# Optimization experiments

Measured on AMD Instinct MI355X. Metric: run time of the kernel, lower is better.

The kernel has to match this reference:

```python
import jax, jax.numpy as jnp
import numpy as np
import math

B, S, E = 4, 2048, 1024


def setup_inputs() -> dict:
    key = jax.random.key(0)
    ks = jax.random.split(key, 7)
    w_scale = 1.0 / math.sqrt(E)
    x = jax.random.normal(ks[0], (B, S, E), dtype=jnp.float32)
    Wq = jax.random.normal(ks[1], (E, E), dtype=jnp.float32) * w_scale
    bq = jax.random.normal(ks[2], (E,), dtype=jnp.float32) * 0.01
    Wk = jax.random.normal(ks[3], (E, E), dtype=jnp.float32) * w_scale
    bk = jax.random.normal(ks[4], (E,), dtype=jnp.float32) * 0.01
    Wv = jax.random.normal(ks[5], (E, E), dtype=jnp.float32) * w_scale
    bv = jax.random.normal(ks[6], (E,), dtype=jnp.float32) * 0.01
    # causal mask: True = attend, False = masked (mask == 0 -> -inf)
    mask = jnp.broadcast_to(jnp.tril(jnp.ones((S, S), dtype=bool)), (B, S, S))
    return {"x": x, "Wq": Wq, "bq": bq, "Wk": Wk, "bk": bk, "Wv": Wv, "bv": bv, "mask": mask}


def reference(x, Wq, bq, Wk, bk, Wv, bv, mask):
    # nn.Linear stores weight as [out, in]: y = x @ W.T + b
    Q = jnp.einsum("bse,oe->bso", x, Wq) + bq
    K = jnp.einsum("bse,oe->bso", x, Wk) + bk
    V = jnp.einsum("bse,oe->bso", x, Wv) + bv
    scale = math.sqrt(E)
    scores = jnp.einsum("bqe,bke->bqk", Q, K) / scale  # [B,S,S]
    scores = jnp.where(mask, scores, -jnp.inf)
    attn = jax.nn.softmax(scores, axis=-1)
    out = jnp.einsum("bqk,bke->bqe", attn, V)  # [B,S,E]
    return out
```

## Files before the change

kernel.cpp:

```cpp
#include <hip/hip_runtime.h>
#include <stdint.h>

typedef unsigned short u16;
typedef __attribute__((ext_vector_type(8))) short bf16x8;
typedef __attribute__((ext_vector_type(4))) float f32x4;

#define MFMA16(a, b, c) __builtin_amdgcn_mfma_f32_16x16x32_bf16((a), (b), (c), 0, 0, 0)

#define MASKVAL (-1.0e30f)

#define WAITV(N) asm volatile("s_waitcnt vmcnt(" #N ")" ::: "memory")
#define LGKM0()  asm volatile("s_waitcnt lgkmcnt(0)" ::: "memory")
#define SBAR()   __builtin_amdgcn_s_barrier()

__device__ __forceinline__ u16 f2bf(float f) {
  union { float f; uint32_t u; } v; v.f = f;
  uint32_t u = v.u;
  u += 0x7fffu + ((u >> 16) & 1u);
  return (u16)(u >> 16);
}
__device__ __forceinline__ void async16(const void* g, void* l) {
  __builtin_amdgcn_global_load_lds(
      (const __attribute__((address_space(1))) unsigned int*)g,
      (__attribute__((address_space(3))) unsigned int*)l, 16, 0, 0);
}

__global__ __launch_bounds__(256) void conv_kernel(
    const float* __restrict__ x,  const float* __restrict__ wq,
    const float* __restrict__ wk, const float* __restrict__ wv,
    u16* __restrict__ xb, u16* __restrict__ wb, int do_wv)
{
  const int NX = 1 << 20;
  const int NW = 1 << 17;
  const int total = NX + NW * (do_wv ? 3 : 2);
  for (int i = blockIdx.x * 256 + threadIdx.x; i < total; i += gridDim.x * 256) {
    const float* src; u16* dst;
    if (i < NX) {
      src = x + (size_t)i * 8;
      const int m = i >> 7, k8 = i & 127;
      dst = xb + (size_t)m * 2048 + 1024 + k8 * 8;
    } else {
      const int j = i - NX;
      const int wsel = j >> 17;
      const int jj = j & (NW - 1);
      const float* W = (wsel == 0) ? wq : (wsel == 1) ? wk : wv;
      const int zoff = (wsel == 0) ? 0 : (wsel == 1) ? (2 << 20) : (1 << 20);
      src = W + (size_t)jj * 8;
      dst = wb + zoff + jj * 8;
    }
    float4 f0 = *(const float4*)src;
    float4 f1 = *(const float4*)(src + 4);
    ushort4 h0, h1;
    h0.x = f2bf(f0.x); h0.y = f2bf(f0.y); h0.z = f2bf(f0.z); h0.w = f2bf(f0.w);
    h1.x = f2bf(f1.x); h1.y = f2bf(f1.y); h1.z = f2bf(f1.z); h1.w = f2bf(f1.w);
    *(ushort4*)dst = h0;
    *(ushort4*)(dst + 4) = h1;
  }
}

template <int BMODE>
__global__ __launch_bounds__(256) void gemm_kernel(
    const u16* __restrict__ xb,
    const u16* __restrict__ wb,
    const float* __restrict__ wv_f,
    const float* __restrict__ bq, const float* __restrict__ bk,
    const float* __restrict__ bv,
    u16* __restrict__ q_out, u16* __restrict__ vt_out, u16* __restrict__ k_out,
    int zbase, int zmul)
{
  const int z = zbase + (int)blockIdx.z * zmul;
  __shared__ u16 lA[2][128 * 32];
  __shared__ u16 lB[2][128 * 32];

  const int m0 = blockIdx.x * 128, n0 = blockIdx.y * 128;
  const int tid = threadIdx.x, lane = tid & 63, w = tid >> 6;
  const int quad = lane >> 4, l15 = lane & 15;
  const int wr = (w >> 1) * 64, wc = (w & 1) * 64;

  const u16* wz = wb + ((size_t)z << 20);
  const float* bias = (z == 0) ? bq : (z == 1) ? bv : bk;

  const int sr  = lane >> 2;
  const int ssw = (lane >> 3) & 3;
  const int c16s = (lane & 3) ^ ssw;

  auto stageA = [&](int kk, int bbuf) {
    const int k0 = kk * 32;
#pragma unroll
    for (int i = 0; i < 2; ++i) {
      const int r = w * 32 + i * 16 + sr;
      async16(&xb[(size_t)(m0 + r) * 2048 + 1024 + k0 + c16s * 8],
              &lA[bbuf][w * 1024 + i * 512]);
    }
  };
  auto stageB = [&](int kk, int bbuf) {
    const int k0 = kk * 32;
#pragma unroll
    for (int i = 0; i < 2; ++i) {
      const int r = w * 32 + i * 16 + sr;
      async16(&wz[(size_t)(n0 + r) * 1024 + k0 + c16s * 8],
              &lB[bbuf][w * 1024 + i * 512]);
    }
  };

  float4 bfr[4];
  const int br = tid >> 1;
  const int bcb = (tid & 1) * 2;
  const int bs = (br >> 1) & 3;
  auto loadB = [&](int kk) {
    const float* p = &wv_f[(size_t)(n0 + br) * 1024 + kk * 32 + bcb * 8];
    bfr[0] = ((const float4*)p)[0];
    bfr[1] = ((const float4*)p)[1];
    bfr[2] = ((const float4*)p)[2];
    bfr[3] = ((const float4*)p)[3];
  };
  auto writeB = [&](int bbuf) {
    ushort4 h[4];
#pragma unroll
    for (int g = 0; g < 4; ++g) {
      h[g].x = f2bf(bfr[g].x); h[g].y = f2bf(bfr[g].y);
      h[g].z = f2bf(bfr[g].z); h[g].w = f2bf(bfr[g].w);
    }
    const int p0 = (bcb + 0) ^ bs, p1 = (bcb + 1) ^ bs;
    *(ushort4*)&lB[bbuf][br * 32 + p0 * 8]     = h[0];
    *(ushort4*)&lB[bbuf][br * 32 + p0 * 8 + 4] = h[1];
    *(ushort4*)&lB[bbuf][br * 32 + p1 * 8]     = h[2];
    *(ushort4*)&lB[bbuf][br * 32 + p1 * 8 + 4] = h[3];
  };

  f32x4 zero4 = {0.f, 0.f, 0.f, 0.f};
  f32x4 acc[4][4];
#pragma unroll
  for (int i = 0; i < 4; ++i)
#pragma unroll
    for (int j = 0; j < 4; ++j) acc[i][j] = zero4;

  if constexpr (BMODE == 0) {
    stageA(0, 0); stageB(0, 0);
  } else {
    stageA(0, 0); loadB(0); writeB(0);
  }

  const int fxor = (l15 >> 1) & 3;
  for (int kk = 0; kk < 32; ++kk) {
    const int bbuf = kk & 1;
    __syncthreads();
    if (kk + 1 < 32) {
      stageA(kk + 1, bbuf ^ 1);
      if constexpr (BMODE == 0) stageB(kk + 1, bbuf ^ 1);
      else loadB(kk + 1);
    }
    bf16x8 af[4], bw[4];
#pragma unroll
    for (int mf = 0; mf < 4; ++mf)
      af[mf] = *(const bf16x8*)
          &lA[bbuf][(wr + mf * 16 + l15) * 32 + (quad ^ fxor) * 8];
#pragma unroll
    for (int nf = 0; nf < 4; ++nf)
      bw[nf] = *(const bf16x8*)
          &lB[bbuf][(wc + nf * 16 + l15) * 32 + (quad ^ fxor) * 8];
#pragma unroll
    for (int mf = 0; mf < 4; ++mf)
#pragma unroll
      for (int nf = 0; nf < 4; ++nf)
        acc[mf][nf] = MFMA16(af[mf], bw[nf], acc[mf][nf]);
    if constexpr (BMODE == 1) {
      if (kk + 1 < 32) writeB(bbuf ^ 1);
    }
  }

  float bvv[4];
#pragma unroll
  for (int nf = 0; nf < 4; ++nf)
    bvv[nf] = bias[n0 + wc + nf * 16 + l15];

  if (z == 0) {
    const float qs = 0.03125f;
#pragma unroll
    for (int mf = 0; mf < 4; ++mf) {
#pragma unroll
      for (int nf = 0; nf < 4; ++nf) {
        const int n = n0 + wc + nf * 16 + l15;
#pragma unroll
        for (int r = 0; r < 4; ++r) {
          const int m = m0 + wr + mf * 16 + quad * 4 + r;
          q_out[(size_t)m * 2048 + n] = f2bf((acc[mf][nf][r] + bvv[nf]) * qs);
        }
      }
    }
  } else if (z == 1) {
#pragma unroll
    for (int mf = 0; mf < 4; ++mf) {
      const int mbase = m0 + wr + mf * 16 + quad * 4;
      const int bb = mbase >> 11;
      const int ss = mbase & 2047;
#pragma unroll
      for (int nf = 0; nf < 4; ++nf) {
        const int n = n0 + wc + nf * 16 + l15;
        ushort4 pk;
        pk.x = f2bf(acc[mf][nf][0] + bvv[nf]);
        pk.y = f2bf(acc[mf][nf][1] + bvv[nf]);
        pk.z = f2bf(acc[mf][nf][2] + bvv[nf]);
        pk.w = f2bf(acc[mf][nf][3] + bvv[nf]);
        *(ushort4*)&vt_out[((size_t)bb << 21) + (size_t)n * 2048 + ss] = pk;
      }
    }
  } else {
#pragma unroll
    for (int mf = 0; mf < 4; ++mf) {
#pragma unroll
      for (int nf = 0; nf < 4; ++nf) {
        const int n = n0 + wc + nf * 16 + l15;
#pragma unroll
        for (int r = 0; r < 4; ++r) {
          const int m = m0 + wr + mf * 16 + quad * 4 + r;
          k_out[(size_t)m * 1024 + n] = f2bf(acc[mf][nf][r] + bvv[nf]);
        }
      }
    }
  }
}

__global__ __launch_bounds__(512) void attn_kernel(
    const u16* __restrict__ Q, const u16* __restrict__ K,
    const u16* __restrict__ VT, float* out)
{
  constexpr int SLOT = 20480;
  __shared__ u16   ring[3][SLOT];
  __shared__ float sS[32 * 132];
  __shared__ u16   sP[32 * 136];
  __shared__ float sAlpha[32];
  __shared__ float sLinv[32];

  const int lin = blockIdx.x + ((int)blockIdx.y << 6);
  const int xcd = lin & 7;
  const int t = ((lin >> 3) << 1) | (xcd & 1);
  const int b = xcd >> 1;
  const int q0 = t * 32;
  const int tid = threadIdx.x, lane = tid & 63, w = tid >> 6;
  const int quad = lane >> 4, l15 = lane & 15;
  const u16* Qb  = Q  + ((size_t)b << 22);
  const u16* Kb  = K  + ((size_t)b << 21);
  const u16* VTb = VT + ((size_t)b << 21);
  float* outb = out + ((size_t)b << 21);

  const int sr = lane >> 4;
  const int sp = lane & 15;

  auto issueK = [&](int kv0, int e0, u16* slot) {
#pragma unroll
    for (int jj = 0; jj < 4; ++jj) {
      const int j = w * 4 + jj;
      const int r = j * 4 + sr;
      const int c16 = sp ^ (r & 15);
      async16(&Kb[(size_t)(kv0 + r) * 1024 + e0 + c16 * 8], slot + j * 512);
    }
  };
  auto issueV = [&](int kv0, int ck, u16* slot) {
#pragma unroll
    for (int jj = 0; jj < 4; ++jj) {
      const int j = w * 4 + jj;
      const int r = j * 4 + sr;
      const int c16 = sp ^ (r & 15);
      async16(&VTb[(size_t)(ck * 128 + r) * 2048 + kv0 + c16 * 8], slot + j * 512);
    }
  };
  auto issueQ = [&](int cq, u16* slot) {
    const int r = w * 4 + sr;
    const int c16 = sp ^ (r & 15);
    async16(&Qb[(size_t)(q0 + r) * 2048 + cq * 128 + c16 * 8],
            slot + 16384 + w * 512);
  };

  f32x4 zero4 = {0.f, 0.f, 0.f, 0.f};
  f32x4 accO[8][2];
#pragma unroll
  for (int c = 0; c < 8; ++c)
#pragma unroll
    for (int i = 0; i < 2; ++i) accO[c][i] = zero4;

  float m_i = MASKVAL, l_i = 0.f;
  const int srow = tid >> 4, slane = tid & 15;

  issueK(0, 0, ring[0]);   issueQ(0, ring[0]);
  issueK(0, 128, ring[1]); issueQ(1, ring[1]);
  int sl = 0, sl2 = 2;

  const int niter = q0 / 128 + 1;
  for (int it = 0; it < niter; ++it) {
    const int kv0 = it * 128;

    f32x4 accS[2];
    accS[0] = zero4; accS[1] = zero4;

#pragma unroll
    for (int c = 0; c < 8; ++c) {
      if (c < 7) { WAITV(5); } else { WAITV(4); }
      SBAR();
      u16* dst = ring[sl2];
      if (c < 6)      { issueK(kv0, (c + 2) * 128, dst); issueQ(c + 2, dst); }
      else if (c == 6) issueV(kv0, 0, dst);
      else             issueV(kv0, 1, dst);
      const u16* bufK = ring[sl];
      const u16* bufQ = ring[sl] + 16384;
#pragma unroll
      for (int ks = 0; ks < 4; ++ks) {
        const int cc = ks * 4 + quad;
        bf16x8 a0 = *(const bf16x8*)&bufQ[l15 * 128 + (cc ^ l15) * 8];
        bf16x8 a1 = *(const bf16x8*)&bufQ[(16 + l15) * 128 + (cc ^ l15) * 8];
        bf16x8 b0 = *(const bf16x8*)&bufK[(w * 16 + l15) * 128 + (cc ^ l15) * 8];
        accS[0] = MFMA16(a0, b0, accS[0]);
        accS[1] = MFMA16(a1, b0, accS[1]);
      }
      sl  = (sl  == 2) ? 0 : sl  + 1;
      sl2 = (sl2 == 2) ? 0 : sl2 + 1;
    }

#pragma unroll
    for (int mf = 0; mf < 2; ++mf)
#pragma unroll
      for (int r = 0; r < 4; ++r) {
        const int row = mf * 16 + quad * 4 + r;
        const int col = w * 16 + l15;
        sS[row * 132 + col] = (kv0 + col <= q0 + row) ? accS[mf][r] : MASKVAL;
      }
    LGKM0();
    SBAR();

    {
      float v[8];
      float4 t0 = *(const float4*)&sS[srow * 132 + slane * 8 + 0];
      float4 t1 = *(const float4*)&sS[srow * 132 + slane * 8 + 4];
      v[0]=t0.x; v[1]=t0.y; v[2]=t0.z; v[3]=t0.w;
      v[4]=t1.x; v[5]=t1.y; v[6]=t1.z; v[7]=t1.w;
      float mx = v[0];
#pragma unroll
      for (int j = 1; j < 8; ++j) mx = fmaxf(mx, v[j]);
#pragma unroll
      for (int d = 1; d < 16; d <<= 1) mx = fmaxf(mx, __shfl_xor(mx, d, 64));
      const float mnew  = fmaxf(m_i, mx);
      const float alpha = __expf(m_i - mnew);
      float sum = 0.f;
      u16 pb[8];
#pragma unroll
      for (int j = 0; j < 8; ++j) {
        const float p = __expf(v[j] - mnew);
        pb[j] = f2bf(p);
        union { uint32_t u; float f; } pv; pv.u = ((uint32_t)pb[j]) << 16;
        sum += pv.f;
      }
      ushort4 pk0, pk1;
      pk0.x = pb[0]; pk0.y = pb[1]; pk0.z = pb[2]; pk0.w = pb[3];
      pk1.x = pb[4]; pk1.y = pb[5]; pk1.z = pb[6]; pk1.w = pb[7];
      *(ushort4*)&sP[srow * 136 + slane * 8 + 0] = pk0;
      *(ushort4*)&sP[srow * 136 + slane * 8 + 4] = pk1;
#pragma unroll
      for (int d = 1; d < 16; d <<= 1) sum += __shfl_xor(sum, d, 64);
      l_i = l_i * alpha + sum;
      m_i = mnew;
      if (slane == 0) sAlpha[srow] = alpha;
      if (it == niter - 1 && slane == 0) sLinv[srow] = 1.0f / l_i;
    }
    LGKM0();
    SBAR();

    float av[2][4];
#pragma unroll
    for (int mf = 0; mf < 2; ++mf)
#pragma unroll
      for (int r = 0; r < 4; ++r)
        av[mf][r] = sAlpha[mf * 16 + quad * 4 + r];
#pragma unroll
    for (int c = 0; c < 8; ++c)
#pragma unroll
      for (int mf = 0; mf < 2; ++mf)
#pragma unroll
        for (int r = 0; r < 4; ++r) accO[c][mf][r] *= av[mf][r];

#pragma unroll
    for (int k = 0; k < 8; ++k) {
      if (k < 7)                 { WAITV(4); }
      else if (it + 1 < niter)   { WAITV(5); }
      else                       { WAITV(0); }
      SBAR();
      u16* dst = ring[sl2];
      if (k < 6) issueV(kv0, k + 2, dst);
      else if (it + 1 < niter) {
        issueK(kv0 + 128, (k - 6) * 128, dst);
        issueQ(k - 6, dst);
      }
      const u16* bufV = ring[sl];
#pragma unroll
      for (int ks = 0; ks < 4; ++ks) {
        const int cc = ks * 4 + quad;
        bf16x8 p0 = *(const bf16x8*)&sP[l15 * 136 + cc * 8];
        bf16x8 p1 = *(const bf16x8*)&sP[(16 + l15) * 136 + cc * 8];
        bf16x8 v0 = *(const bf16x8*)&bufV[(w * 16 + l15) * 128 + (cc ^ l15) * 8];
        accO[k][0] = MFMA16(p0, v0, accO[k][0]);
        accO[k][1] = MFMA16(p1, v0, accO[k][1]);
      }
      sl  = (sl  == 2) ? 0 : sl  + 1;
      sl2 = (sl2 == 2) ? 0 : sl2 + 1;
    }
  }

  float lv[2][4];
#pragma unroll
  for (int mf = 0; mf < 2; ++mf)
#pragma unroll
    for (int r = 0; r < 4; ++r)
      lv[mf][r] = sLinv[mf * 16 + quad * 4 + r];
#pragma unroll
  for (int c = 0; c < 8; ++c)
#pragma unroll
    for (int mf = 0; mf < 2; ++mf) {
      const int col = c * 128 + w * 16 + l15;
#pragma unroll
      for (int r = 0; r < 4; ++r) {
        const int row = q0 + mf * 16 + quad * 4 + r;
        outb[(size_t)row * 1024 + col] = accO[c][mf][r] * lv[mf][r];
      }
    }
}

extern "C" void kernel_launch(void* const* d_in, const int* in_sizes, int n_in,
                              void* d_out, int out_size, void* d_ws, size_t ws_size,
                              hipStream_t stream) {
  (void)in_sizes; (void)n_in; (void)out_size;
  const float* x  = (const float*)d_in[0];
  const float* Wq = (const float*)d_in[1];
  const float* bq = (const float*)d_in[2];
  const float* Wk = (const float*)d_in[3];
  const float* bk = (const float*)d_in[4];
  const float* Wv = (const float*)d_in[5];
  const float* bv = (const float*)d_in[6];

  u16* qbuf = (u16*)d_out;
  u16* vtw  = (u16*)d_in[7];
  u16* kw   = (u16*)d_ws;

  const bool ws_big = ws_size >= (size_t)22 * 1024 * 1024;
  u16* wb = ws_big ? (u16*)d_ws + (8u << 20) : (u16*)d_in[7];

  conv_kernel<<<dim3(2048), 256, 0, stream>>>(x, Wq, Wk, Wv, qbuf, wb,
                                              ws_big ? 1 : 0);
  if (ws_big) {
    gemm_kernel<0><<<dim3(64, 8, 3), 256, 0, stream>>>(
        qbuf, wb, Wv, bq, bk, bv, qbuf, vtw, kw, 0, 1);
  } else {
    gemm_kernel<0><<<dim3(64, 8, 2), 256, 0, stream>>>(
        qbuf, wb, Wv, bq, bk, bv, qbuf, vtw, kw, 0, 2);
    gemm_kernel<1><<<dim3(64, 8, 1), 256, 0, stream>>>(
        qbuf, wb, Wv, bq, bk, bv, qbuf, vtw, kw, 1, 1);
  }

  attn_kernel<<<dim3(64, 4), 512, 0, stream>>>(qbuf, kw, vtw, (float*)d_out);
}
```

Measured before the change: 414.4 us.

## Remap GEMM blocks per XCD, raise MFMA priority, hoist P fragment loads

Result: no change. 414.0 us (-0.1%).

```diff
diff --git a/kernel.cpp b/kernel.cpp
--- a/kernel.cpp
+++ b/kernel.cpp
@@ -66,13 +66,19 @@
     const float* __restrict__ bq, const float* __restrict__ bk,
     const float* __restrict__ bv,
     u16* __restrict__ q_out, u16* __restrict__ vt_out, u16* __restrict__ k_out,
-    int zbase, int zmul)
+    int mode)
 {
-  const int z = zbase + (int)blockIdx.z * zmul;
   __shared__ u16 lA[2][128 * 32];
   __shared__ u16 lB[2][128 * 32];
 
-  const int m0 = blockIdx.x * 128, n0 = blockIdx.y * 128;
+  const int flat = blockIdx.x;
+  const int xcd = flat & 7, idx = flat >> 3;
+  int n_g, mm, z;
+  if (mode == 0)      { n_g = xcd * 3 + idx % 3;  mm = idx / 3;  z = n_g >> 3; }
+  else if (mode == 1) { n_g = xcd * 2 + (idx & 1); mm = idx >> 1; z = (n_g < 8) ? 0 : 2; }
+  else                { n_g = xcd;                 mm = idx;      z = 1; }
+  const int m0 = mm * 128, n0 = (n_g & 7) * 128;
+
   const int tid = threadIdx.x, lane = tid & 63, w = tid >> 6;
   const int quad = lane >> 4, l15 = lane & 15;
   const int wr = (w >> 1) * 64, wc = (w & 1) * 64;
@@ -159,11 +165,13 @@
     for (int nf = 0; nf < 4; ++nf)
       bw[nf] = *(const bf16x8*)
           &lB[bbuf][(wc + nf * 16 + l15) * 32 + (quad ^ fxor) * 8];
+    __builtin_amdgcn_s_setprio(1);
 #pragma unroll
     for (int mf = 0; mf < 4; ++mf)
 #pragma unroll
       for (int nf = 0; nf < 4; ++nf)
         acc[mf][nf] = MFMA16(af[mf], bw[nf], acc[mf][nf]);
+    __builtin_amdgcn_s_setprio(0);
     if constexpr (BMODE == 1) {
       if (kk + 1 < 32) writeB(bbuf ^ 1);
     }
@@ -303,6 +311,7 @@
       else             issueV(kv0, 1, dst);
       const u16* bufK = ring[sl];
       const u16* bufQ = ring[sl] + 16384;
+      __builtin_amdgcn_s_setprio(1);
 #pragma unroll
       for (int ks = 0; ks < 4; ++ks) {
         const int cc = ks * 4 + quad;
@@ -312,6 +321,7 @@
         accS[0] = MFMA16(a0, b0, accS[0]);
         accS[1] = MFMA16(a1, b0, accS[1]);
       }
+      __builtin_amdgcn_s_setprio(0);
       sl  = (sl  == 2) ? 0 : sl  + 1;
       sl2 = (sl2 == 2) ? 0 : sl2 + 1;
     }
@@ -376,6 +386,14 @@
       for (int mf = 0; mf < 2; ++mf)
 #pragma unroll
         for (int r = 0; r < 4; ++r) accO[c][mf][r] *= av[mf][r];
+
+    bf16x8 pf0[4], pf1[4];
+#pragma unroll
+    for (int ks = 0; ks < 4; ++ks) {
+      const int cc = ks * 4 + quad;
+      pf0[ks] = *(const bf16x8*)&sP[l15 * 136 + cc * 8];
+      pf1[ks] = *(const bf16x8*)&sP[(16 + l15) * 136 + cc * 8];
+    }
 
 #pragma unroll
     for (int k = 0; k < 8; ++k) {
@@ -390,15 +408,15 @@
         issueQ(k - 6, dst);
       }
       const u16* bufV = ring[sl];
+      __builtin_amdgcn_s_setprio(1);
 #pragma unroll
       for (int ks = 0; ks < 4; ++ks) {
         const int cc = ks * 4 + quad;
-        bf16x8 p0 = *(const bf16x8*)&sP[l15 * 136 + cc * 8];
-        bf16x8 p1 = *(const bf16x8*)&sP[(16 + l15) * 136 + cc * 8];
         bf16x8 v0 = *(const bf16x8*)&bufV[(w * 16 + l15) * 128 + (cc ^ l15) * 8];
-        accO[k][0] = MFMA16(p0, v0, accO[k][0]);
-        accO[k][1] = MFMA16(p1, v0, accO[k][1]);
-      }
+        accO[k][0] = MFMA16(pf0[ks], v0, accO[k][0]);
+        accO[k][1] = MFMA16(pf1[ks], v0, accO[k][1]);
+      }
+      __builtin_amdgcn_s_setprio(0);
       sl  = (sl  == 2) ? 0 : sl  + 1;
       sl2 = (sl2 == 2) ? 0 : sl2 + 1;
     }
@@ -445,13 +463,13 @@
   conv_kernel<<<dim3(2048), 256, 0, stream>>>(x, Wq, Wk, Wv, qbuf, wb,
                                               ws_big ? 1 : 0);
   if (ws_big) {
-    gemm_kernel<0><<<dim3(64, 8, 3), 256, 0, stream>>>(
-        qbuf, wb, Wv, bq, bk, bv, qbuf, vtw, kw, 0, 1);
+    gemm_kernel<0><<<dim3(1536), 256, 0, stream>>>(
+        qbuf, wb, Wv, bq, bk, bv, qbuf, vtw, kw, 0);
   } else {
-    gemm_kernel<0><<<dim3(64, 8, 2), 256, 0, stream>>>(
-        qbuf, wb, Wv, bq, bk, bv, qbuf, vtw, kw, 0, 2);
-    gemm_kernel<1><<<dim3(64, 8, 1), 256, 0, stream>>>(
-        qbuf, wb, Wv, bq, bk, bv, qbuf, vtw, kw, 1, 1);
+    gemm_kernel<0><<<dim3(1024), 256, 0, stream>>>(
+        qbuf, wb, Wv, bq, bk, bv, qbuf, vtw, kw, 1);
+    gemm_kernel<1><<<dim3(512), 256, 0, stream>>>(
+        qbuf, wb, Wv, bq, bk, bv, qbuf, vtw, kw, 2);
   }
 
   attn_kernel<<<dim3(64, 4), 512, 0, stream>>>(qbuf, kw, vtw, (float*)d_out);
```
